# Optimization experiments

Hardware: AMD Instinct MI355X
Metric: run time of the kernel (lower is better)

Reference implementation:

```python
import jax, jax.numpy as jnp
import numpy as np

N = 4096      # nodes
DIM = 256     # in/out channels
H = 8         # heads
C = DIM       # per-head channels (PyG TransformerConv: out_channels per head)
EPS = 1e-5    # LayerNorm eps
P_EDGE = 0.01 # adjacency density -> avg in-degree ~41


def setup_inputs() -> dict:
    key = jax.random.key(0)
    ks = jax.random.split(key, 12)
    x = jax.random.normal(ks[0], (1, N, DIM), jnp.float32)
    # sparse random graph encoded densely (dense_to_sparse extracts nonzeros)
    adj_mat = (jax.random.uniform(ks[1], (1, N, N)) < P_EDGE).astype(jnp.float32)
    s = 1.0 / np.sqrt(DIM)
    Wq = jax.random.normal(ks[2], (DIM, H * C), jnp.float32) * s
    Wk = jax.random.normal(ks[3], (DIM, H * C), jnp.float32) * s
    Wv = jax.random.normal(ks[4], (DIM, H * C), jnp.float32) * s
    bq = jax.random.normal(ks[5], (H * C,), jnp.float32) * 0.01
    bk = jax.random.normal(ks[6], (H * C,), jnp.float32) * 0.01
    bv = jax.random.normal(ks[7], (H * C,), jnp.float32) * 0.01
    Wskip = jax.random.normal(ks[8], (DIM, DIM), jnp.float32) * s
    bskip = jax.random.normal(ks[9], (DIM,), jnp.float32) * 0.01
    gamma = jnp.ones((DIM,), jnp.float32)
    beta = jnp.zeros((DIM,), jnp.float32)
    return dict(x=x, adj_mat=adj_mat, Wq=Wq, bq=bq, Wk=Wk, bk=bk, Wv=Wv, bv=bv,
                Wskip=Wskip, bskip=bskip, gamma=gamma, beta=beta)


def reference(x, adj_mat, Wq, bq, Wk, bk, Wv, bv, Wskip, bskip, gamma, beta):
    xs = x[0]            # [N, DIM]
    adj = adj_mat[0]     # [N, N]; adj[j, i] != 0 => edge j -> i (source_to_target)
    q = (xs @ Wq + bq).reshape(N, H, C)
    k = (xs @ Wk + bk).reshape(N, H, C)
    v = (xs @ Wv + bv).reshape(N, H, C)
    # scaled dot-product attention restricted to graph edges
    scores = jnp.einsum('ihc,jhc->hij', q, k) / jnp.sqrt(jnp.float32(C))  # [H,N,N]
    mask = (adj.T != 0.0)[None]  # [1, i_target, j_source]
    neg = jnp.finfo(scores.dtype).min
    attn = jax.nn.softmax(jnp.where(mask, scores, neg), axis=-1)
    # nodes with no in-edges aggregate zero messages (scatter semantics)
    has_nbr = mask.any(axis=-1, keepdims=True)  # [1, N, 1]
    attn = jnp.where(has_nbr, attn, 0.0)
    agg = jnp.einsum('hij,jhc->ihc', attn, v)  # [N, H, C]
    out = agg.mean(axis=1)                      # concat=False -> head mean, [N, DIM]
    out = out + xs @ Wskip + bskip              # root_weight skip connection
    mu = out.mean(axis=-1, keepdims=True)
    var = ((out - mu) ** 2).mean(axis=-1, keepdims=True)
    out = (out - mu) * jax.lax.rsqrt(var + EPS) * gamma + beta  # LayerNorm
    out = out + xs                               # residual
    return out[None]  # [1, N, DIM]
```

## Files before the change

kernel.cpp:

```cpp
#include <hip/hip_runtime.h>
#include <hip/hip_bf16.h>

#define NN   4096
#define DIMM 256
#define HH   8
#define HC   2048
#define CAP  128

#define QSCALE 15.875f
#define SSCALE (0.0625f / (QSCALE * QSCALE))
#define V4SCALE 1.75f
#define V4INV  (4.0f / 7.0f)
#define V4CORR (32.0f / 7.0f)

typedef short    bf16x8 __attribute__((ext_vector_type(8)));
typedef float    f32x4  __attribute__((ext_vector_type(4)));

__device__ __forceinline__ unsigned short f2bf(float f) {
  union { float f; unsigned int u; } un; un.f = f;
  unsigned int r = un.u + 0x7fffu + ((un.u >> 16) & 1u);
  return (unsigned short)(r >> 16);
}
__device__ __forceinline__ int sdot4(unsigned int a, unsigned int b, int c) {
#if __has_builtin(__builtin_amdgcn_sdot4)
  return __builtin_amdgcn_sdot4((int)a, (int)b, c, false);
#else
  c += (int)(signed char)(a)       * (int)(signed char)(b);
  c += (int)(signed char)(a >> 8)  * (int)(signed char)(b >> 8);
  c += (int)(signed char)(a >> 16) * (int)(signed char)(b >> 16);
  c += (int)(signed char)(a >> 24) * (int)(signed char)(b >> 24);
  return c;
#endif
}
__device__ __forceinline__ void gload16(const void* g, void* l) {
  __builtin_amdgcn_global_load_lds(
      (const __attribute__((address_space(1))) unsigned int*)g,
      (__attribute__((address_space(3))) unsigned int*)l, 16, 0, 0);
}
__device__ __forceinline__ unsigned int pack8n(unsigned int a, unsigned int b) {
  const unsigned int ya = a | (a >> 4);
  const unsigned int yb = b | (b >> 4);
  return (ya & 0xFFu) | ((ya >> 8) & 0xFF00u) |
         (((yb & 0xFFu) | ((yb >> 8) & 0xFF00u)) << 16);
}

__global__ __launch_bounds__(256) void build_edges_kernel(
    const float4* __restrict__ adj4, int* __restrict__ deg, int* __restrict__ nbr) {
  const int stride = gridDim.x * blockDim.x;
  for (int e4 = blockIdx.x * blockDim.x + threadIdx.x; e4 < NN * NN / 4; e4 += stride) {
    const float4 a = adj4[e4];
    if (a.x != 0.f || a.y != 0.f || a.z != 0.f || a.w != 0.f) {
      const int e = e4 << 2;
      const int j = e >> 12;
      const int ib = e & (NN - 1);
      if (a.x != 0.f) { int s = atomicAdd(&deg[ib + 0], 1); if (s < CAP) nbr[(ib + 0) * CAP + s] = j; }
      if (a.y != 0.f) { int s = atomicAdd(&deg[ib + 1], 1); if (s < CAP) nbr[(ib + 1) * CAP + s] = j; }
      if (a.z != 0.f) { int s = atomicAdd(&deg[ib + 2], 1); if (s < CAP) nbr[(ib + 2) * CAP + s] = j; }
      if (a.w != 0.f) { int s = atomicAdd(&deg[ib + 3], 1); if (s < CAP) nbr[(ib + 3) * CAP + s] = j; }
    }
  }
}

__global__ __launch_bounds__(128) void sort_nbr_kernel(
    const int* __restrict__ deg, int* __restrict__ nbr) {
  const int i = blockIdx.x, t = threadIdx.x;
  __shared__ int sl[CAP];
  int d = deg[i];
  if (d > CAP) d = CAP;
  if (d <= 1) return;
  sl[t] = (t < d) ? nbr[i * CAP + t] : 0x7fffffff;
  __syncthreads();
  for (int ksz = 2; ksz <= CAP; ksz <<= 1) {
    for (int jsz = ksz >> 1; jsz > 0; jsz >>= 1) {
      const int ixj = t ^ jsz;
      if (ixj > t) {
        const int a = sl[t], b = sl[ixj];
        const bool up = ((t & ksz) == 0);
        if ((up && a > b) || (!up && a < b)) { sl[t] = b; sl[ixj] = a; }
      }
      __syncthreads();
    }
  }
  if (t < d) nbr[i * CAP + t] = sl[t];
}

__global__ __launch_bounds__(256) void cast_x_kernel(
    const float* __restrict__ x, unsigned short* __restrict__ xb,
    int* __restrict__ deg) {
  if (blockIdx.x < 16) deg[blockIdx.x * 256 + threadIdx.x] = 0;
  const int gid = blockIdx.x * 256 + threadIdx.x;
  const int m = gid >> 5, c = gid & 31;
  const float4 a = *(const float4*)&x[(size_t)m * 256 + c * 8];
  const float4 b = *(const float4*)&x[(size_t)m * 256 + c * 8 + 4];
  union { unsigned short u[8]; uint4 v; } o;
  o.u[0] = f2bf(a.x); o.u[1] = f2bf(a.y); o.u[2] = f2bf(a.z); o.u[3] = f2bf(a.w);
  o.u[4] = f2bf(b.x); o.u[5] = f2bf(b.y); o.u[6] = f2bf(b.z); o.u[7] = f2bf(b.w);
  const int cs = (c & 24) | ((c & 7) ^ (m & 7));
  *(uint4*)&xb[(size_t)m * 256 + cs * 8] = o.v;
}

__global__ __launch_bounds__(256) void tcast_w_kernel(
    const float* __restrict__ W0, const float* __restrict__ W1,
    const float* __restrict__ W2, const float* __restrict__ W3,
    unsigned short* __restrict__ T0, unsigned short* __restrict__ T1,
    unsigned short* __restrict__ T2, unsigned short* __restrict__ T3) {
  const int z = blockIdx.z;
  if (z == 3 && blockIdx.x >= 4) return;
  const float* W = z == 0 ? W0 : z == 1 ? W1 : z == 2 ? W2 : W3;
  unsigned short* T = z == 0 ? T0 : z == 1 ? T1 : z == 2 ? T2 : T3;
  const int Nw = (z == 3) ? 256 : 2048;
  __shared__ float Tf[64][68];
  const int t = threadIdx.x;
  const int n0 = blockIdx.x * 64, k0 = blockIdx.y * 64;
  const int kk0 = t >> 4, nc = t & 15;
#pragma unroll
  for (int r = 0; r < 4; ++r) {
    const int kk = kk0 + r * 16;
    const float4 a = *(const float4*)&W[(size_t)(k0 + kk) * Nw + n0 + nc * 4];
    Tf[kk][nc * 4 + 0] = a.x; Tf[kk][nc * 4 + 1] = a.y;
    Tf[kk][nc * 4 + 2] = a.z; Tf[kk][nc * 4 + 3] = a.w;
  }
  __syncthreads();
  const int n = t >> 2, cp = t & 3;
#pragma unroll
  for (int qq = 0; qq < 2; ++qq) {
    const int cc = cp * 2 + qq;
    union { unsigned short u[8]; uint4 v; } o;
#pragma unroll
    for (int e = 0; e < 8; ++e) o.u[e] = f2bf(Tf[cc * 8 + e][n]);
    const int ng = n0 + n;
    const int co = cc ^ (ng & 7);
    *(uint4*)&T[(size_t)ng * 256 + blockIdx.y * 64 + co * 8] = o.v;
  }
}

__global__ __launch_bounds__(256) void mfma_gemm_kernel(
    const unsigned short* __restrict__ Abf,
    const unsigned short* __restrict__ B0, const unsigned short* __restrict__ B1,
    const unsigned short* __restrict__ B2, const unsigned short* __restrict__ B3,
    const float* __restrict__ bias0, const float* __restrict__ bias1,
    const float* __restrict__ bias2, const float* __restrict__ bias3,
    void* __restrict__ C0v, void* __restrict__ C1v,
    void* __restrict__ C2v, void* __restrict__ C3v) {
  const int z = blockIdx.z;
  if (z == 3 && blockIdx.x >= 2) return;
  const unsigned short* Bm = z == 0 ? B0 : z == 1 ? B1 : z == 2 ? B2 : B3;
  const float* bias = z == 0 ? bias0 : z == 1 ? bias1 : z == 2 ? bias2 : bias3;
  void* Cv = z == 0 ? C0v : z == 1 ? C1v : z == 2 ? C2v : C3v;
  const int Nc = (z == 3) ? 256 : 2048;

  __shared__ unsigned short lds[2 * 128 * 64];
  unsigned short* As = lds;
  unsigned short* Bs = lds + 128 * 64;

  const int t = threadIdx.x, l = t & 63, w = t >> 6;
  const int m0 = blockIdx.y * 128, n0 = blockIdx.x * 128;
  const int wm = w >> 1, wn = w & 1;

  const f32x4 zero = {0.f, 0.f, 0.f, 0.f};
  f32x4 acc[4][4];
#pragma unroll
  for (int fm = 0; fm < 4; ++fm)
#pragma unroll
    for (int fn = 0; fn < 4; ++fn) acc[fm][fn] = zero;

  for (int kb = 0; kb < 4; ++kb) {
#pragma unroll
    for (int r = 0; r < 4; ++r) {
      const int rr = r * 8 + (l >> 3), ch = l & 7;
      gload16(Abf + (size_t)(m0 + w * 32 + rr) * 256 + kb * 64 + ch * 8,
              As + w * 2048 + r * 512);
      gload16(Bm + (size_t)(n0 + w * 32 + rr) * 256 + kb * 64 + ch * 8,
              Bs + w * 2048 + r * 512);
    }
    __syncthreads();

#pragma unroll
    for (int s = 0; s < 2; ++s) {
      const int chab = (4 * s + (l >> 4)) ^ (l & 7);
      bf16x8 af[4], bfr[4];
#pragma unroll
      for (int fm = 0; fm < 4; ++fm) {
        const int row = wm * 64 + fm * 16 + (l & 15);
        af[fm] = *(const bf16x8*)&As[row * 64 + chab * 8];
      }
#pragma unroll
      for (int fn = 0; fn < 4; ++fn) {
        const int row = wn * 64 + fn * 16 + (l & 15);
        bfr[fn] = *(const bf16x8*)&Bs[row * 64 + chab * 8];
      }
#pragma unroll
      for (int fm = 0; fm < 4; ++fm)
#pragma unroll
        for (int fn = 0; fn < 4; ++fn)
          acc[fm][fn] = __builtin_amdgcn_mfma_f32_16x16x32_bf16(
              af[fm], bfr[fn], acc[fm][fn], 0, 0, 0);
    }
    __syncthreads();
  }

  float bv[4];
#pragma unroll
  for (int fn = 0; fn < 4; ++fn) bv[fn] = bias[n0 + wn * 64 + fn * 16 + (l & 15)];

  if (z < 2) {
    unsigned char* lds8 = (unsigned char*)lds;
    unsigned char* Cc8 = (unsigned char*)Cv;
#pragma unroll
    for (int fm = 0; fm < 4; ++fm) {
      const int col = wn * 64 + (l & 15);
#pragma unroll
      for (int fn = 0; fn < 4; ++fn) {
#pragma unroll
        for (int r = 0; r < 4; ++r) {
          const int row = wm * 64 + fm * 16 + (l >> 4) * 4 + r;
          const float val = acc[fm][fn][r] + bv[fn];
          int vi = (int)rintf(val * QSCALE);
          vi = vi < -127 ? -127 : (vi > 127 ? 127 : vi);
          lds8[row * 128 + col + fn * 16] = (unsigned char)(signed char)vi;
        }
      }
    }
    __syncthreads();
#pragma unroll
    for (int r2 = 0; r2 < 4; ++r2) {
      const int idx = r2 * 256 + t;
      const int row = idx >> 3, colb = (idx & 7) * 16;
      *(uint4*)&Cc8[(size_t)(m0 + row) * Nc + n0 + colb] =
          *(const uint4*)&lds8[row * 128 + colb];
    }
  } else if (z == 2) {
    unsigned char* lds8 = (unsigned char*)lds;
    unsigned char* Cc8 = (unsigned char*)Cv;
#pragma unroll
    for (int fm = 0; fm < 4; ++fm) {
      const int col = wn * 64 + (l & 15);
#pragma unroll
      for (int fn = 0; fn < 4; ++fn) {
#pragma unroll
        for (int r = 0; r < 4; ++r) {
          const int row = wm * 64 + fm * 16 + (l >> 4) * 4 + r;
          const float val = acc[fm][fn][r] + bv[fn];
          int vi = (int)rintf(val * V4SCALE) + 8;
          vi = vi < 0 ? 0 : (vi > 15 ? 15 : vi);
          lds8[row * 128 + col + fn * 16] = (unsigned char)vi;
        }
      }
    }
    __syncthreads();
    const int hd = n0 >> 8, g2 = hd >> 2, hrel = hd & 3;
    const int c8base = (n0 & 255) >> 3;
#pragma unroll
    for (int u = 0; u < 8; ++u) {
      const int unit = u * 256 + t;
      const int row = unit >> 4, c8r = unit & 15;
      const uint2 x0 = *(const uint2*)&lds8[row * 128 + c8r * 8];
      const unsigned int pk = pack8n(x0.x, x0.y);
      *(unsigned int*)&Cc8[(size_t)(m0 + row) * 1024 + g2 * 512 +
                           (c8base + c8r) * 16 + hrel * 4] = pk;
    }
  } else {
    float* Cc = (float*)Cv;
#pragma unroll
    for (int fm = 0; fm < 4; ++fm)
#pragma unroll
      for (int fn = 0; fn < 4; ++fn)
#pragma unroll
        for (int r = 0; r < 4; ++r) {
          const int row = wm * 64 + fm * 16 + (l >> 4) * 4 + r;
          const int col = wn * 64 + fn * 16 + (l & 15);
          Cc[(size_t)(m0 + row) * Nc + n0 + col] = acc[fm][fn][r] + bv[fn];
        }
  }
}

__global__ __launch_bounds__(256) void attn_ln_kernel(
    const unsigned char* __restrict__ q8, const unsigned char* __restrict__ k8,
    const unsigned char* __restrict__ v4, const float* __restrict__ skip,
    const float* __restrict__ x, const int* __restrict__ deg,
    const int* __restrict__ nbr, const float* __restrict__ gamma,
    const float* __restrict__ beta, float* __restrict__ out) {
  const int i = blockIdx.x;
  const int t = threadIdx.x;
  const int lane = t & 63, wave = t >> 6;
  const int h = lane >> 3, sub = lane & 7;

  __shared__ int slist[CAP];
  __shared__ float sc[CAP * HH];
  __shared__ float wacc[4][2][DIMM];
  __shared__ float mred[HH], lred[HH];
  __shared__ float w1[4], w2[4];

  int d = deg[i];
  if (d > CAP) d = CAP;

  if (t < CAP) slist[t] = (t < d) ? nbr[i * CAP + t] : 0;

  uint4 Q0, Q1;
  {
    const uint4* qp = (const uint4*)&q8[(size_t)i * HC + (h << 8) + (sub << 5)];
    Q0 = qp[0]; Q1 = qp[1];
  }
  __syncthreads();

  {
    const size_t hoff = (size_t)(h << 8) + (sub << 5);
    int n = wave;
    uint4 a0, a1, b0, b1;
    if (n < d) {
      const uint4* kp = (const uint4*)&k8[(size_t)slist[n] * HC + hoff];
      a0 = kp[0]; a1 = kp[1];
    }
    if (n + 4 < d) {
      const uint4* kp = (const uint4*)&k8[(size_t)slist[n + 4] * HC + hoff];
      b0 = kp[0]; b1 = kp[1];
    }
    while (n < d) {
      uint4 c0, c1;
      if (n + 8 < d) {
        const uint4* kp = (const uint4*)&k8[(size_t)slist[n + 8] * HC + hoff];
        c0 = kp[0]; c1 = kp[1];
      }
      int iacc = 0;
      iacc = sdot4(a0.x, Q0.x, iacc); iacc = sdot4(a0.y, Q0.y, iacc);
      iacc = sdot4(a0.z, Q0.z, iacc); iacc = sdot4(a0.w, Q0.w, iacc);
      iacc = sdot4(a1.x, Q1.x, iacc); iacc = sdot4(a1.y, Q1.y, iacc);
      iacc = sdot4(a1.z, Q1.z, iacc); iacc = sdot4(a1.w, Q1.w, iacc);
      float s = (float)iacc;
      s += __shfl_xor(s, 1);
      s += __shfl_xor(s, 2);
      s += __shfl_xor(s, 4);
      if (sub == 0) sc[n * HH + h] = s * SSCALE;
      a0 = b0; a1 = b1; b0 = c0; b1 = c1;
      n += 4;
    }
  }
  __syncthreads();

  if (t < 64) {
    const int h2i = t >> 3, s2 = t & 7;
    float m = -1e30f;
    for (int n2 = s2; n2 < d; n2 += 8) m = fmaxf(m, sc[n2 * HH + h2i]);
    m = fmaxf(m, __shfl_xor(m, 1));
    m = fmaxf(m, __shfl_xor(m, 2));
    m = fmaxf(m, __shfl_xor(m, 4));
    float lsum = 0.f;
    for (int n2 = s2; n2 < d; n2 += 8) lsum += expf(sc[n2 * HH + h2i] - m);
    lsum += __shfl_xor(lsum, 1);
    lsum += __shfl_xor(lsum, 2);
    lsum += __shfl_xor(lsum, 4);
    if (s2 == 0) { mred[h2i] = m; lred[h2i] = (lsum > 0.f) ? V4INV / lsum : 0.f; }
  }
  __syncthreads();

  for (int e = t; e < d * HH; e += 256) {
    const int hh = e & (HH - 1);
    sc[e] = expf(sc[e] - mred[hh]) * lred[hh];
  }
  __syncthreads();

  float a[8] = {0.f, 0.f, 0.f, 0.f, 0.f, 0.f, 0.f, 0.f};
  const int g = lane >> 5, c8 = lane & 31;
  {
    const size_t voff = (size_t)g * 512 + (size_t)c8 * 16;
    int n = wave;
    uint4 A, B, C;
    if (n < d)     A = *(const uint4*)&v4[(size_t)slist[n] * 1024 + voff];
    if (n + 4 < d) B = *(const uint4*)&v4[(size_t)slist[n + 4] * 1024 + voff];
    if (n + 8 < d) C = *(const uint4*)&v4[(size_t)slist[n + 8] * 1024 + voff];
    while (n < d) {
      uint4 Dw;
      if (n + 12 < d) Dw = *(const uint4*)&v4[(size_t)slist[n + 12] * 1024 + voff];
      const float p0 = sc[n * HH + g * 4 + 0];
      const float p1 = sc[n * HH + g * 4 + 1];
      const float p2 = sc[n * HH + g * 4 + 2];
      const float p3 = sc[n * HH + g * 4 + 3];
#define AGG4(w, p)                                                     \
      {                                                                \
        const unsigned int lo = (w) & 0x0F0F0F0Fu;                     \
        const unsigned int hi = ((w) >> 4) & 0x0F0F0F0Fu;              \
        a[0] = fmaf(p, (float)(lo & 0xFFu), a[0]);                     \
        a[1] = fmaf(p, (float)(hi & 0xFFu), a[1]);                     \
        a[2] = fmaf(p, (float)((lo >> 8) & 0xFFu), a[2]);              \
        a[3] = fmaf(p, (float)((hi >> 8) & 0xFFu), a[3]);              \
        a[4] = fmaf(p, (float)((lo >> 16) & 0xFFu), a[4]);             \
        a[5] = fmaf(p, (float)((hi >> 16) & 0xFFu), a[5]);             \
        a[6] = fmaf(p, (float)(lo >> 24), a[6]);                       \
        a[7] = fmaf(p, (float)(hi >> 24), a[7]);                       \
      }
      AGG4(A.x, p0) AGG4(A.y, p1) AGG4(A.z, p2) AGG4(A.w, p3)
#undef AGG4
      A = B; B = C; C = Dw;
      n += 4;
    }
  }
#pragma unroll
  for (int e = 0; e < 8; ++e) wacc[wave][g][c8 * 8 + e] = a[e];
  __syncthreads();

  float accsum = 0.f;
#pragma unroll
  for (int w2 = 0; w2 < 4; ++w2) accsum += wacc[w2][0][t] + wacc[w2][1][t];
  const float corr = (d > 0) ? V4CORR : 0.f;
  const float oval = accsum * 0.125f - corr + skip[(size_t)i * DIMM + t];

  float s1 = oval, s2 = oval * oval;
#pragma unroll
  for (int off = 32; off > 0; off >>= 1) {
    s1 += __shfl_xor(s1, off, 64);
    s2 += __shfl_xor(s2, off, 64);
  }
  if (lane == 0) { w1[wave] = s1; w2[wave] = s2; }
  __syncthreads();
  const float S1 = w1[0] + w1[1] + w1[2] + w1[3];
  const float S2 = w2[0] + w2[1] + w2[2] + w2[3];
  const float mu = S1 * (1.0f / 256.0f);
  const float var = S2 * (1.0f / 256.0f) - mu * mu;
  const float rst = rsqrtf(var + 1e-5f);

  out[(size_t)i * DIMM + t] =
      (oval - mu) * rst * gamma[t] + beta[t] + x[(size_t)i * DIMM + t];
}

extern "C" void kernel_launch(void* const* d_in, const int* in_sizes, int n_in,
                              void* d_out, int out_size, void* d_ws, size_t ws_size,
                              hipStream_t stream) {
  const float* x     = (const float*)d_in[0];
  const float* adj   = (const float*)d_in[1];
  const float* Wq    = (const float*)d_in[2];
  const float* bq    = (const float*)d_in[3];
  const float* Wk    = (const float*)d_in[4];
  const float* bk    = (const float*)d_in[5];
  const float* Wv    = (const float*)d_in[6];
  const float* bv    = (const float*)d_in[7];
  const float* Wskip = (const float*)d_in[8];
  const float* bskip = (const float*)d_in[9];
  const float* gamma = (const float*)d_in[10];
  const float* beta  = (const float*)d_in[11];
  float* out = (float*)d_out;

  char* ws = (char*)d_ws;
  unsigned short* xb  = (unsigned short*)ws;
  unsigned short* WqT = xb  + (size_t)NN * DIMM;
  unsigned short* WkT = WqT + (size_t)HC * DIMM;
  unsigned short* WvT = WkT + (size_t)HC * DIMM;
  unsigned short* WsT = WvT + (size_t)HC * DIMM;
  float* skip = (float*)(WsT + (size_t)DIMM * DIMM);
  unsigned char* q8 = (unsigned char*)(skip + (size_t)NN * DIMM);
  unsigned char* k8 = q8 + (size_t)NN * HC;
  unsigned char* v4 = k8 + (size_t)NN * HC;
  int* deg = (int*)(v4 + (size_t)NN * 1024);
  int* nbr = deg + NN;

  cast_x_kernel<<<NN * 32 / 256, 256, 0, stream>>>(x, xb, deg);
  build_edges_kernel<<<2048, 256, 0, stream>>>((const float4*)adj, deg, nbr);
  sort_nbr_kernel<<<NN, 128, 0, stream>>>(deg, nbr);

  tcast_w_kernel<<<dim3(HC / 64, 4, 4), 256, 0, stream>>>(
      Wq, Wk, Wv, Wskip, WqT, WkT, WvT, WsT);

  mfma_gemm_kernel<<<dim3(HC / 128, NN / 128, 4), 256, 0, stream>>>(
      xb, WqT, WkT, WvT, WsT, bq, bk, bv, bskip, q8, k8, v4, skip);

  attn_ln_kernel<<<NN, 256, 0, stream>>>(q8, k8, v4, skip, x, deg, nbr,
                                         gamma, beta, out);
}
```

Measured before the change: 136.8 us.

## Fuse score, softmax and aggregation into a single online-softmax pass

Replaces the separate score pass, shared-memory softmax and value-aggregation pass with one loop per wave that computes scores, keeps a running max and sum per head with lazy rescaling, and accumulates values at the same time. Per-wave partial maxima and sums are then merged across the four waves through shared memory. This removes two barriers, the score buffer in shared memory and a second gather loop over neighbours, while K and V loads are prefetched together. In exchange each thread keeps 32 accumulators plus running state, which adds register pressure, and the lazy rescale threshold of 8 allows exponentials up to e^8 before renormalising.

```diff
diff --git a/kernel.cpp b/kernel.cpp
--- a/kernel.cpp
+++ b/kernel.cpp
@@ -283,12 +283,11 @@
   const int i = blockIdx.x;
   const int t = threadIdx.x;
   const int lane = t & 63, wave = t >> 6;
-  const int h = lane >> 3, sub = lane & 7;
+  const int g = lane >> 5, c8 = lane & 31;
 
   __shared__ int slist[CAP];
-  __shared__ float sc[CAP * HH];
+  __shared__ float wm[4][2][4], wl[4][2][4];
   __shared__ float wacc[4][2][DIMM];
-  __shared__ float mred[HH], lred[HH];
   __shared__ float w1[4], w2[4];
 
   int d = deg[i];
@@ -298,104 +297,110 @@
 
   uint4 Q0, Q1;
   {
-    const uint4* qp = (const uint4*)&q8[(size_t)i * HC + (h << 8) + (sub << 5)];
+    const uint4* qp = (const uint4*)&q8[(size_t)i * HC + (size_t)lane * 32];
     Q0 = qp[0]; Q1 = qp[1];
   }
   __syncthreads();
 
+  float mh[4] = {-1e30f, -1e30f, -1e30f, -1e30f};
+  float lh[4] = {0.f, 0.f, 0.f, 0.f};
+  float acc[4][8] = {};
   {
-    const size_t hoff = (size_t)(h << 8) + (sub << 5);
+    const size_t koff = (size_t)lane * 32;
+    const size_t voff = (size_t)g * 512 + (size_t)c8 * 16;
     int n = wave;
-    uint4 a0, a1, b0, b1;
+    uint4 ka0, ka1, va, kb0, kb1, vb;
     if (n < d) {
-      const uint4* kp = (const uint4*)&k8[(size_t)slist[n] * HC + hoff];
-      a0 = kp[0]; a1 = kp[1];
+      const int j = slist[n];
+      const uint4* kp = (const uint4*)&k8[(size_t)j * HC + koff];
+      ka0 = kp[0]; ka1 = kp[1];
+      va = *(const uint4*)&v4[(size_t)j * 1024 + voff];
     }
     if (n + 4 < d) {
-      const uint4* kp = (const uint4*)&k8[(size_t)slist[n + 4] * HC + hoff];
-      b0 = kp[0]; b1 = kp[1];
+      const int j = slist[n + 4];
+      const uint4* kp = (const uint4*)&k8[(size_t)j * HC + koff];
+      kb0 = kp[0]; kb1 = kp[1];
+      vb = *(const uint4*)&v4[(size_t)j * 1024 + voff];
     }
     while (n < d) {
-      uint4 c0, c1;
+      uint4 kc0, kc1, vc;
       if (n + 8 < d) {
-        const uint4* kp = (const uint4*)&k8[(size_t)slist[n + 8] * HC + hoff];
-        c0 = kp[0]; c1 = kp[1];
+        const int j = slist[n + 8];
+        const uint4* kp = (const uint4*)&k8[(size_t)j * HC + koff];
+        kc0 = kp[0]; kc1 = kp[1];
+        vc = *(const uint4*)&v4[(size_t)j * 1024 + voff];
       }
       int iacc = 0;
-      iacc = sdot4(a0.x, Q0.x, iacc); iacc = sdot4(a0.y, Q0.y, iacc);
-      iacc = sdot4(a0.z, Q0.z, iacc); iacc = sdot4(a0.w, Q0.w, iacc);
-      iacc = sdot4(a1.x, Q1.x, iacc); iacc = sdot4(a1.y, Q1.y, iacc);
-      iacc = sdot4(a1.z, Q1.z, iacc); iacc = sdot4(a1.w, Q1.w, iacc);
+      iacc = sdot4(ka0.x, Q0.x, iacc); iacc = sdot4(ka0.y, Q0.y, iacc);
+      iacc = sdot4(ka0.z, Q0.z, iacc); iacc = sdot4(ka0.w, Q0.w, iacc);
+      iacc = sdot4(ka1.x, Q1.x, iacc); iacc = sdot4(ka1.y, Q1.y, iacc);
+      iacc = sdot4(ka1.z, Q1.z, iacc); iacc = sdot4(ka1.w, Q1.w, iacc);
       float s = (float)iacc;
       s += __shfl_xor(s, 1);
       s += __shfl_xor(s, 2);
       s += __shfl_xor(s, 4);
-      if (sub == 0) sc[n * HH + h] = s * SSCALE;
-      a0 = b0; a1 = b1; b0 = c0; b1 = c1;
-      n += 4;
-    }
-  }
-  __syncthreads();
-
-  if (t < 64) {
-    const int h2i = t >> 3, s2 = t & 7;
-    float m = -1e30f;
-    for (int n2 = s2; n2 < d; n2 += 8) m = fmaxf(m, sc[n2 * HH + h2i]);
-    m = fmaxf(m, __shfl_xor(m, 1));
-    m = fmaxf(m, __shfl_xor(m, 2));
-    m = fmaxf(m, __shfl_xor(m, 4));
-    float lsum = 0.f;
-    for (int n2 = s2; n2 < d; n2 += 8) lsum += expf(sc[n2 * HH + h2i] - m);
-    lsum += __shfl_xor(lsum, 1);
-    lsum += __shfl_xor(lsum, 2);
-    lsum += __shfl_xor(lsum, 4);
-    if (s2 == 0) { mred[h2i] = m; lred[h2i] = (lsum > 0.f) ? V4INV / lsum : 0.f; }
-  }
-  __syncthreads();
-
-  for (int e = t; e < d * HH; e += 256) {
-    const int hh = e & (HH - 1);
-    sc[e] = expf(sc[e] - mred[hh]) * lred[hh];
-  }
-  __syncthreads();
-
-  float a[8] = {0.f, 0.f, 0.f, 0.f, 0.f, 0.f, 0.f, 0.f};
-  const int g = lane >> 5, c8 = lane & 31;
-  {
-    const size_t voff = (size_t)g * 512 + (size_t)c8 * 16;
-    int n = wave;
-    uint4 A, B, C;
-    if (n < d)     A = *(const uint4*)&v4[(size_t)slist[n] * 1024 + voff];
-    if (n + 4 < d) B = *(const uint4*)&v4[(size_t)slist[n + 4] * 1024 + voff];
-    if (n + 8 < d) C = *(const uint4*)&v4[(size_t)slist[n + 8] * 1024 + voff];
-    while (n < d) {
-      uint4 Dw;
-      if (n + 12 < d) Dw = *(const uint4*)&v4[(size_t)slist[n + 12] * 1024 + voff];
-      const float p0 = sc[n * HH + g * 4 + 0];
-      const float p1 = sc[n * HH + g * 4 + 1];
-      const float p2 = sc[n * HH + g * 4 + 2];
-      const float p3 = sc[n * HH + g * 4 + 3];
-#define AGG4(w, p)                                                     \
+      s *= SSCALE;
+      float sv[4], P[4];
+#pragma unroll
+      for (int j2 = 0; j2 < 4; ++j2)
+        sv[j2] = __shfl(s, ((g << 2) + j2) << 3);
+#pragma unroll
+      for (int j2 = 0; j2 < 4; ++j2) {
+        const float sj = sv[j2];
+        if (sj > mh[j2] + 8.0f) {
+          const float r = __expf(mh[j2] - sj);
+          lh[j2] *= r;
+#pragma unroll
+          for (int e = 0; e < 8; ++e) acc[j2][e] *= r;
+          mh[j2] = sj;
+        }
+        P[j2] = __expf(sj - mh[j2]);
+        lh[j2] += P[j2];
+      }
+#define AGG4(w, p, ar)                                                 \
       {                                                                \
         const unsigned int lo = (w) & 0x0F0F0F0Fu;                     \
         const unsigned int hi = ((w) >> 4) & 0x0F0F0F0Fu;              \
-        a[0] = fmaf(p, (float)(lo & 0xFFu), a[0]);                     \
-        a[1] = fmaf(p, (float)(hi & 0xFFu), a[1]);                     \
-        a[2] = fmaf(p, (float)((lo >> 8) & 0xFFu), a[2]);              \
-        a[3] = fmaf(p, (float)((hi >> 8) & 0xFFu), a[3]);              \
-        a[4] = fmaf(p, (float)((lo >> 16) & 0xFFu), a[4]);             \
-        a[5] = fmaf(p, (float)((hi >> 16) & 0xFFu), a[5]);             \
-        a[6] = fmaf(p, (float)(lo >> 24), a[6]);                       \
-        a[7] = fmaf(p, (float)(hi >> 24), a[7]);                       \
-      }
-      AGG4(A.x, p0) AGG4(A.y, p1) AGG4(A.z, p2) AGG4(A.w, p3)
+        ar[0] = fmaf(p, (float)(lo & 0xFFu), ar[0]);                   \
+        ar[1] = fmaf(p, (float)(hi & 0xFFu), ar[1]);                   \
+        ar[2] = fmaf(p, (float)((lo >> 8) & 0xFFu), ar[2]);            \
+        ar[3] = fmaf(p, (float)((hi >> 8) & 0xFFu), ar[3]);            \
+        ar[4] = fmaf(p, (float)((lo >> 16) & 0xFFu), ar[4]);           \
+        ar[5] = fmaf(p, (float)((hi >> 16) & 0xFFu), ar[5]);           \
+        ar[6] = fmaf(p, (float)(lo >> 24), ar[6]);                     \
+        ar[7] = fmaf(p, (float)(hi >> 24), ar[7]);                     \
+      }
+      AGG4(va.x, P[0], acc[0]) AGG4(va.y, P[1], acc[1])
+      AGG4(va.z, P[2], acc[2]) AGG4(va.w, P[3], acc[3])
 #undef AGG4
-      A = B; B = C; C = Dw;
+      ka0 = kb0; ka1 = kb1; va = vb;
+      kb0 = kc0; kb1 = kc1; vb = vc;
       n += 4;
     }
   }
-#pragma unroll
-  for (int e = 0; e < 8; ++e) wacc[wave][g][c8 * 8 + e] = a[e];
+
+  if (c8 == 0) {
+#pragma unroll
+    for (int j2 = 0; j2 < 4; ++j2) {
+      wm[wave][g][j2] = mh[j2];
+      wl[wave][g][j2] = lh[j2];
+    }
+  }
+  __syncthreads();
+  float f[4];
+#pragma unroll
+  for (int j2 = 0; j2 < 4; ++j2) {
+    const float m0v = wm[0][g][j2], m1v = wm[1][g][j2];
+    const float m2v = wm[2][g][j2], m3v = wm[3][g][j2];
+    const float M = fmaxf(fmaxf(m0v, m1v), fmaxf(m2v, m3v));
+    const float L = wl[0][g][j2] * __expf(m0v - M) + wl[1][g][j2] * __expf(m1v - M) +
+                    wl[2][g][j2] * __expf(m2v - M) + wl[3][g][j2] * __expf(m3v - M);
+    f[j2] = (L > 0.f) ? V4INV * __expf(mh[j2] - M) / L : 0.f;
+  }
+#pragma unroll
+  for (int e = 0; e < 8; ++e)
+    wacc[wave][g][c8 * 8 + e] = acc[0][e] * f[0] + acc[1][e] * f[1] +
+                                acc[2][e] * f[2] + acc[3][e] * f[3];
   __syncthreads();
 
   float accsum = 0.f;
```

New measurement: 144.8 us. 5.8% more time.
